# Kernel optimization log

Measured on AMD Instinct MI355X. Metric: run time of the kernel, lower is better.

Reference implementation:

```python
import jax, jax.numpy as jnp
import numpy as np

THRESH = 0.7
MIN_KEPT = 100000
IGNORE_INDEX = -100


def setup_inputs() -> dict:
    key = jax.random.key(0)
    k1, k2 = jax.random.split(key)
    B, C, H, W = 8, 19, 512, 512
    logits = jax.random.normal(k1, (B, C, H, W), dtype=jnp.float32)
    targets = jax.random.randint(k2, (B, H, W), 0, C, dtype=jnp.int64)
    return {"logits": logits, "targets": targets}


def reference(logits, targets):
    B, C, H, W = logits.shape
    # softmax over class dim, then log(p + eps) as in the original
    probs = jax.nn.softmax(logits, axis=1)
    log_probs = jnp.log(probs + 1e-7)
    mask = (targets != IGNORE_INDEX)
    # per-pixel NLL: gather log-prob of the target class
    gathered = jnp.take_along_axis(log_probs, targets[:, None, :, :], axis=1)[:, 0]  # [B,H,W]
    losses = -gathered * mask.astype(logits.dtype)                                   # [B,H,W]
    losses_flat = losses.reshape(B, -1)                                              # [B,HW]
    n_pix = losses_flat.shape[1]
    # threshold index is static (Python ints), matching torch code exactly
    thresh_idx = max(MIN_KEPT, int(n_pix * THRESH))
    thresh_idx = min(thresh_idx, n_pix - 1)
    sorted_losses = jnp.sort(losses_flat, axis=1)
    thresh = sorted_losses[:, thresh_idx]                                            # [B]
    selected = losses_flat > thresh[:, None]                                         # [B,HW] bool
    # Faithful to the original (buggy-looking) loop:
    #   selected_mask[i, targets[i].flatten()] = 1
    # i.e. target *values* are used as indices into the flattened HW axis.
    tgt_flat = targets.reshape(B, -1)  # values in [0, C)
    selected = jax.vmap(lambda s, t: s.at[t].set(True))(selected, tgt_flat)
    return selected.reshape(B, H, W).astype(jnp.float32)
```

## Files before the change

kernel.cpp:

```cpp
#include <hip/hip_runtime.h>

#define NB 8
#define NC 19
#define HW (512*512)
#define NPIX (NB*HW)
#define RANK 183500u
#define NBIN 4096
#define CAPL 4096

__device__ __forceinline__ unsigned fkey(float f) {
    unsigned b = __float_as_uint(f);
    return (b & 0x80000000u) ? ~b : (b | 0x80000000u);
}
__device__ __forceinline__ float finv(unsigned u) {
    unsigned b = (u & 0x80000000u) ? (u & 0x7fffffffu) : ~u;
    return __uint_as_float(b);
}
__device__ __forceinline__ int bin_of(float l) {
    int b = (int)((l + 1.0f) * 224.0f);
    return b < 0 ? 0 : (b > NBIN - 1 ? NBIN - 1 : b);
}
__device__ __forceinline__ unsigned umn(unsigned a, unsigned b) { return a < b ? a : b; }
__device__ __forceinline__ unsigned umx(unsigned a, unsigned b) { return a > b ? a : b; }

__global__ __launch_bounds__(256) void losses_kernel(
    const float* __restrict__ logits, const int* __restrict__ targets,
    float* __restrict__ losses, unsigned* __restrict__ present,
    unsigned* __restrict__ ghist)
{
    __shared__ unsigned pres;
    const int blk  = blockIdx.x;
    const int pix0 = blk * 512;
    const int bb   = pix0 >> 18;
    const int pp   = pix0 & (HW - 1);
    const int tid  = threadIdx.x;

    if (tid == 0) pres = 0u;
    if (blk < 32)
        for (int j = tid; j < 1024; j += 256) ghist[blk * 1024 + j] = 0u;

    const float* base = logits + (size_t)bb * NC * HW + pp + tid * 2;
    float2 x[NC];
    #pragma unroll
    for (int c = 0; c < NC; ++c)
        x[c] = *reinterpret_cast<const float2*>(base + (size_t)c * HW);

    int2 t = *reinterpret_cast<const int2*>(targets + pix0 + tid * 2);

    float m0 = x[0].x, m1 = x[0].y;
    #pragma unroll
    for (int c = 1; c < NC; ++c) { m0 = fmaxf(m0, x[c].x); m1 = fmaxf(m1, x[c].y); }

    float s0 = 0.f, s1 = 0.f, e0t = 0.f, e1t = 0.f;
    #pragma unroll
    for (int c = 0; c < NC; ++c) {
        float e0 = expf(x[c].x - m0); s0 += e0; if (c == t.x) e0t = e0;
        float e1 = expf(x[c].y - m1); s1 += e1; if (c == t.y) e1t = e1;
    }
    float o0 = 0.f, o1 = 0.f;
    unsigned mbit = 0u;
    if (t.x >= 0 && t.x < NC) { o0 = -logf(e0t / s0 + 1e-7f); mbit |= 1u << t.x; }
    if (t.y >= 0 && t.y < NC) { o1 = -logf(e1t / s1 + 1e-7f); mbit |= 1u << t.y; }
    *reinterpret_cast<float2*>(losses + pix0 + tid * 2) = make_float2(o0, o1);

    #pragma unroll
    for (int o = 1; o < 64; o <<= 1) mbit |= __shfl_xor(mbit, o);
    __syncthreads();
    if ((tid & 63) == 0 && mbit) atomicOr(&pres, mbit);
    __syncthreads();
    if (tid == 0 && pres) atomicOr(&present[bb], pres);
}

__global__ __launch_bounds__(256) void hist_kernel(
    const float* __restrict__ losses, unsigned* __restrict__ ghist)
{
    __shared__ unsigned lh[NBIN];
    const int b = blockIdx.y;
    for (int j = threadIdx.x; j < NBIN; j += 256) lh[j] = 0;
    __syncthreads();
    const float4* L = reinterpret_cast<const float4*>(losses + (size_t)b * HW)
                      + (size_t)blockIdx.x * 1024;
    for (int j = threadIdx.x; j < 1024; j += 256) {
        float4 v = L[j];
        atomicAdd(&lh[bin_of(v.x)], 1u);
        atomicAdd(&lh[bin_of(v.y)], 1u);
        atomicAdd(&lh[bin_of(v.z)], 1u);
        atomicAdd(&lh[bin_of(v.w)], 1u);
    }
    __syncthreads();
    unsigned* gh = ghist + b * NBIN;
    for (int j = threadIdx.x; j < NBIN; j += 256) {
        unsigned v = lh[j];
        if (v) atomicAdd(&gh[j], v);
    }
}

__global__ __launch_bounds__(1024) void select_kernel(
    const float* __restrict__ losses, const unsigned* __restrict__ ghist,
    float* __restrict__ thresh)
{
    __shared__ unsigned lh[NBIN];
    __shared__ unsigned cand[CAPL];
    __shared__ unsigned hsub[512];
    __shared__ unsigned wsum[16], woff[16], redmin[16], redmax[16];
    __shared__ unsigned sh_bin, sh_r, sh_cnt, sh_kmin, sh_shift, sh_sb, sh_r2;

    const int b = blockIdx.x, tid = threadIdx.x;
    const int lane = tid & 63, wid = tid >> 6;

    for (int j = tid; j < NBIN; j += 1024) lh[j] = ghist[b * NBIN + j];
    if (tid == 0) sh_cnt = 0;
    __syncthreads();

    unsigned s = lh[tid * 4] + lh[tid * 4 + 1] + lh[tid * 4 + 2] + lh[tid * 4 + 3];
    unsigned incl = s;
    #pragma unroll
    for (int o = 1; o < 64; o <<= 1) {
        unsigned v = (unsigned)__shfl_up((int)incl, o);
        if (lane >= o) incl += v;
    }
    if (lane == 63) wsum[wid] = incl;
    __syncthreads();
    if (tid == 0) { unsigned c = 0; for (int w = 0; w < 16; ++w) { woff[w] = c; c += wsum[w]; } }
    __syncthreads();
    unsigned excl = woff[wid] + incl - s;
    if (RANK >= excl && RANK < excl + s) {
        unsigned rr = RANK - excl, cum = 0;
        #pragma unroll
        for (int j = 0; j < 4; ++j) {
            unsigned c = lh[tid * 4 + j];
            if (cum + c > rr) { sh_bin = (unsigned)(tid * 4 + j); sh_r = rr - cum; break; }
            cum += c;
        }
    }
    __syncthreads();
    const int T = (int)sh_bin;
    const unsigned r = sh_r;

    const float4* L = reinterpret_cast<const float4*>(losses + (size_t)b * HW);
    for (int j = tid; j < HW / 4; j += 1024) {
        float4 v = L[j];
        if (bin_of(v.x) == T) { unsigned i = atomicAdd(&sh_cnt, 1u); if (i < CAPL) cand[i] = fkey(v.x); }
        if (bin_of(v.y) == T) { unsigned i = atomicAdd(&sh_cnt, 1u); if (i < CAPL) cand[i] = fkey(v.y); }
        if (bin_of(v.z) == T) { unsigned i = atomicAdd(&sh_cnt, 1u); if (i < CAPL) cand[i] = fkey(v.z); }
        if (bin_of(v.w) == T) { unsigned i = atomicAdd(&sh_cnt, 1u); if (i < CAPL) cand[i] = fkey(v.w); }
    }
    __syncthreads();
    unsigned k = sh_cnt; if (k > CAPL) k = CAPL;

    unsigned lmin = 0xFFFFFFFFu, lmax = 0u;
    for (unsigned j = tid; j < k; j += 1024) { unsigned v = cand[j]; lmin = umn(lmin, v); lmax = umx(lmax, v); }
    #pragma unroll
    for (int o = 1; o < 64; o <<= 1) {
        lmin = umn(lmin, (unsigned)__shfl_xor((int)lmin, o));
        lmax = umx(lmax, (unsigned)__shfl_xor((int)lmax, o));
    }
    if (lane == 0) { redmin[wid] = lmin; redmax[wid] = lmax; }
    if (tid < 512) hsub[tid] = 0;
    __syncthreads();
    if (tid == 0) {
        unsigned mn = redmin[0], mx = redmax[0];
        for (int w = 1; w < 16; ++w) { mn = umn(mn, redmin[w]); mx = umx(mx, redmax[w]); }
        unsigned spread = mx - mn;
        int bits = 32 - __clz((int)(spread | 1u));
        sh_shift = (unsigned)(bits > 9 ? bits - 9 : 0);
        sh_kmin = mn;
    }
    __syncthreads();
    const unsigned kmin = sh_kmin, shift = sh_shift;
    for (unsigned j = tid; j < k; j += 1024) atomicAdd(&hsub[(cand[j] - kmin) >> shift], 1u);
    __syncthreads();

    unsigned s2 = (tid < 512) ? hsub[tid] : 0u;
    unsigned incl2 = s2;
    #pragma unroll
    for (int o = 1; o < 64; o <<= 1) {
        unsigned v = (unsigned)__shfl_up((int)incl2, o);
        if (lane >= o) incl2 += v;
    }
    if (lane == 63) wsum[wid] = incl2;
    __syncthreads();
    if (tid == 0) { unsigned c = 0; for (int w = 0; w < 16; ++w) { woff[w] = c; c += wsum[w]; } }
    __syncthreads();
    unsigned excl2 = woff[wid] + incl2 - s2;
    if (tid < 512 && s2 && r >= excl2 && r < excl2 + s2) { sh_sb = (unsigned)tid; sh_r2 = r - excl2; }
    __syncthreads();
    const unsigned sb = sh_sb;

    for (unsigned j = tid; j < k; j += 1024) {
        unsigned v = cand[j];
        if (((v - kmin) >> shift) != sb) continue;
        unsigned less = 0, eq = 0;
        for (unsigned q = 0; q < k; ++q) {
            unsigned u = cand[q];
            less += (u < v);
            eq   += (u == v);
        }
        if (less <= r && r < less + eq) thresh[b] = finv(v);
    }
}

__global__ __launch_bounds__(256) void emit_kernel(
    float* __restrict__ out, const float* __restrict__ thresh,
    const unsigned* __restrict__ present)
{
    int i4 = blockIdx.x * 256 + threadIdx.x;
    int i = i4 * 4;
    int b = i >> 18;
    int p = i & (HW - 1);
    float th = thresh[b];
    unsigned pm = present[b];
    float4 v = reinterpret_cast<float4*>(out)[i4];
    float4 o;
    o.x = ((v.x > th) || ((p + 0) < NC && ((pm >> (p + 0)) & 1u))) ? 1.f : 0.f;
    o.y = ((v.y > th) || ((p + 1) < NC && ((pm >> (p + 1)) & 1u))) ? 1.f : 0.f;
    o.z = ((v.z > th) || ((p + 2) < NC && ((pm >> (p + 2)) & 1u))) ? 1.f : 0.f;
    o.w = ((v.w > th) || ((p + 3) < NC && ((pm >> (p + 3)) & 1u))) ? 1.f : 0.f;
    reinterpret_cast<float4*>(out)[i4] = o;
}

extern "C" void kernel_launch(void* const* d_in, const int* in_sizes, int n_in,
                              void* d_out, int out_size, void* d_ws, size_t ws_size,
                              hipStream_t stream)
{
    const float* logits  = (const float*)d_in[0];
    const int*   targets = (const int*)d_in[1];
    float* out = (float*)d_out;

    char* ws = (char*)d_ws;
    unsigned* present = (unsigned*)(ws);
    float*    thresh  = (float*)   (ws + 32);
    unsigned* ghist   = (unsigned*)(ws + 64);

    hipMemsetAsync(present, 0, 32, stream);

    losses_kernel<<<NPIX / 512, 256, 0, stream>>>(logits, targets, out, present, ghist);
    hist_kernel<<<dim3(64, NB), 256, 0, stream>>>(out, ghist);
    select_kernel<<<NB, 1024, 0, stream>>>(out, ghist, thresh);
    emit_kernel<<<NPIX / 4 / 256, 256, 0, stream>>>(out, thresh, present);
}
```

Before: 130.4 us.

## Fuse loss histogram into the loss kernel and drop separate hist pass

```diff
diff --git a/kernel.cpp b/kernel.cpp
--- a/kernel.cpp
+++ b/kernel.cpp
@@ -28,71 +28,54 @@
     float* __restrict__ losses, unsigned* __restrict__ present,
     unsigned* __restrict__ ghist)
 {
+    __shared__ unsigned lh[NBIN];
     __shared__ unsigned pres;
-    const int blk  = blockIdx.x;
-    const int pix0 = blk * 512;
-    const int bb   = pix0 >> 18;
-    const int pp   = pix0 & (HW - 1);
-    const int tid  = threadIdx.x;
+    const int blk = blockIdx.x;
+    const int bb  = (blk * 256) >> 18;
+    const int pp  = (blk * 256) & (HW - 1);
+    const int tid = threadIdx.x;
 
     if (tid == 0) pres = 0u;
-    if (blk < 32)
-        for (int j = tid; j < 1024; j += 256) ghist[blk * 1024 + j] = 0u;
-
-    const float* base = logits + (size_t)bb * NC * HW + pp + tid * 2;
-    float2 x[NC];
-    #pragma unroll
-    for (int c = 0; c < NC; ++c)
-        x[c] = *reinterpret_cast<const float2*>(base + (size_t)c * HW);
-
-    int2 t = *reinterpret_cast<const int2*>(targets + pix0 + tid * 2);
-
-    float m0 = x[0].x, m1 = x[0].y;
-    #pragma unroll
-    for (int c = 1; c < NC; ++c) { m0 = fmaxf(m0, x[c].x); m1 = fmaxf(m1, x[c].y); }
-
-    float s0 = 0.f, s1 = 0.f, e0t = 0.f, e1t = 0.f;
+    for (int j = tid; j < NBIN; j += 256) lh[j] = 0u;
+
+    const float* base = logits + (size_t)bb * NC * HW + pp + tid;
+
+    float x[NC];
+    #pragma unroll
+    for (int c = 0; c < NC; ++c) x[c] = base[(size_t)c * HW];
+
+    const int t = targets[blk * 256 + tid];
+
+    float m = x[0];
+    #pragma unroll
+    for (int c = 1; c < NC; ++c) m = fmaxf(m, x[c]);
+
+    float s = 0.f, et = 0.f;
     #pragma unroll
     for (int c = 0; c < NC; ++c) {
-        float e0 = expf(x[c].x - m0); s0 += e0; if (c == t.x) e0t = e0;
-        float e1 = expf(x[c].y - m1); s1 += e1; if (c == t.y) e1t = e1;
-    }
-    float o0 = 0.f, o1 = 0.f;
+        float e = expf(x[c] - m);
+        s += e;
+        if (c == t) et = e;
+    }
+    float o = 0.f;
     unsigned mbit = 0u;
-    if (t.x >= 0 && t.x < NC) { o0 = -logf(e0t / s0 + 1e-7f); mbit |= 1u << t.x; }
-    if (t.y >= 0 && t.y < NC) { o1 = -logf(e1t / s1 + 1e-7f); mbit |= 1u << t.y; }
-    *reinterpret_cast<float2*>(losses + pix0 + tid * 2) = make_float2(o0, o1);
-
-    #pragma unroll
-    for (int o = 1; o < 64; o <<= 1) mbit |= __shfl_xor(mbit, o);
-    __syncthreads();
+    if (t >= 0 && t < NC) { o = -logf(et / s + 1e-7f); mbit = 1u << t; }
+    losses[blk * 256 + tid] = o;
+
+    #pragma unroll
+    for (int off = 1; off < 64; off <<= 1) mbit |= __shfl_xor(mbit, off);
+
+    __syncthreads();
+    atomicAdd(&lh[bin_of(o)], 1u);
     if ((tid & 63) == 0 && mbit) atomicOr(&pres, mbit);
     __syncthreads();
-    if (tid == 0 && pres) atomicOr(&present[bb], pres);
-}
-
-__global__ __launch_bounds__(256) void hist_kernel(
-    const float* __restrict__ losses, unsigned* __restrict__ ghist)
-{
-    __shared__ unsigned lh[NBIN];
-    const int b = blockIdx.y;
-    for (int j = threadIdx.x; j < NBIN; j += 256) lh[j] = 0;
-    __syncthreads();
-    const float4* L = reinterpret_cast<const float4*>(losses + (size_t)b * HW)
-                      + (size_t)blockIdx.x * 1024;
-    for (int j = threadIdx.x; j < 1024; j += 256) {
-        float4 v = L[j];
-        atomicAdd(&lh[bin_of(v.x)], 1u);
-        atomicAdd(&lh[bin_of(v.y)], 1u);
-        atomicAdd(&lh[bin_of(v.z)], 1u);
-        atomicAdd(&lh[bin_of(v.w)], 1u);
-    }
-    __syncthreads();
-    unsigned* gh = ghist + b * NBIN;
-    for (int j = threadIdx.x; j < NBIN; j += 256) {
+
+    unsigned* gh = ghist + bb * NBIN;
+    for (int j = tid; j < NBIN; j += 256) {
         unsigned v = lh[j];
         if (v) atomicAdd(&gh[j], v);
     }
+    if (tid == 0 && pres) atomicOr(&present[bb], pres);
 }
 
 __global__ __launch_bounds__(1024) void select_kernel(
@@ -232,10 +215,9 @@
     float*    thresh  = (float*)   (ws + 32);
     unsigned* ghist   = (unsigned*)(ws + 64);
 
-    hipMemsetAsync(present, 0, 32, stream);
-
-    losses_kernel<<<NPIX / 512, 256, 0, stream>>>(logits, targets, out, present, ghist);
-    hist_kernel<<<dim3(64, NB), 256, 0, stream>>>(out, ghist);
+    hipMemsetAsync(ws, 0, 64 + NB * NBIN * sizeof(unsigned), stream);
+
+    losses_kernel<<<NPIX / 256, 256, 0, stream>>>(logits, targets, out, present, ghist);
     select_kernel<<<NB, 1024, 0, stream>>>(out, ghist, thresh);
     emit_kernel<<<NPIX / 4 / 256, 256, 0, stream>>>(out, thresh, present);
 }
```

New measurement: 171.6 us. +31.6%, slower.
